# Optimization experiments

Hardware: AMD Instinct MI355X
Metric: run time of the kernel (lower is better)

## Reference

```python
import jax, jax.numpy as jnp
import numpy as np

N_NODES = 100000
N_EDGES = 1000000
S = 64      # n_hidden_scalars
F = 64      # n_hidden_edge_feats
RBF = 16    # rbf_dim
V = 16      # n_vec_channels
IN_DIM = 2 * S + F + RBF  # 208, EdgeUpdate MLP input


def _layernorm(x, g, b):
    m = x.mean(-1, keepdims=True)
    var = ((x - m) ** 2).mean(-1, keepdims=True)
    return (x - m) / jnp.sqrt(var + 1e-5) * g + b


def _gvp(s, v, Wh, Wu, Ws, bs, sigmoid_gate):
    # s: [N, S]; v: [N, v_in, 3]
    vh = jnp.einsum('nvc,vh->nhc', v, Wh)          # [N, h, 3]
    vu = jnp.einsum('nhc,hu->nuc', vh, Wu)          # [N, v_out, 3]
    sh = jnp.sqrt(jnp.sum(vh * vh, axis=-1) + 1e-8)  # [N, h]
    s_out = jax.nn.silu(jnp.concatenate([s, sh], axis=-1) @ Ws + bs)
    vn = jnp.sqrt(jnp.sum(vu * vu, axis=-1, keepdims=True) + 1e-8)  # [N, v_out, 1]
    gate = jax.nn.sigmoid(vn) if sigmoid_gate else vn
    return s_out, gate * vu


def setup_inputs() -> dict:
    key = jax.random.key(0)
    ks = jax.random.split(key, 24)

    def nrm(k, shape, fan_in):
        return jax.random.normal(k, shape, dtype=jnp.float32) / np.sqrt(fan_in)

    inp = {
        'node_scalars': jax.random.normal(ks[0], (N_NODES, S), dtype=jnp.float32),
        'positions': jax.random.normal(ks[1], (N_NODES, 3), dtype=jnp.float32),
        'vectors': jax.random.normal(ks[2], (N_NODES, V, 3), dtype=jnp.float32),
        'edge_feats': jax.random.normal(ks[3], (N_EDGES, F), dtype=jnp.float32),
        'd': jax.random.uniform(ks[4], (N_EDGES, RBF), dtype=jnp.float32),
        'src_idx': jax.random.randint(ks[5], (N_EDGES,), 0, N_NODES, dtype=jnp.int32),
        'dst_idx': jax.random.randint(ks[6], (N_EDGES,), 0, N_NODES, dtype=jnp.int32),
        # EdgeUpdate MLP + LayerNorm params
        'W1': nrm(ks[7], (IN_DIM, F), IN_DIM), 'b1': jnp.zeros((F,), jnp.float32),
        'W2': nrm(ks[8], (F, F), F),           'b2': jnp.zeros((F,), jnp.float32),
        'ln_g': jnp.ones((F,), jnp.float32),   'ln_b': jnp.zeros((F,), jnp.float32),
        # GVP 0: s 64->64, v 16->16 (h=16), sigmoid vector gate
        'gvp0_Wh': nrm(ks[9], (V, V), V), 'gvp0_Wu': nrm(ks[10], (V, V), V),
        'gvp0_Ws': nrm(ks[11], (S + V, S), S + V), 'gvp0_bs': jnp.zeros((S,), jnp.float32),
        # GVP 1: same shapes
        'gvp1_Wh': nrm(ks[12], (V, V), V), 'gvp1_Wu': nrm(ks[13], (V, V), V),
        'gvp1_Ws': nrm(ks[14], (S + V, S), S + V), 'gvp1_bs': jnp.zeros((S,), jnp.float32),
        # GVP 2 (last): v 16->1, identity vector activation
        'gvp2_Wh': nrm(ks[15], (V, V), V), 'gvp2_Wu': nrm(ks[16], (V, 1), V),
        'gvp2_Ws': nrm(ks[17], (S + V, S), S + V), 'gvp2_bs': jnp.zeros((S,), jnp.float32),
    }
    return inp


def reference(node_scalars, positions, vectors, edge_feats, d, src_idx, dst_idx,
              W1, b1, W2, b2, ln_g, ln_b,
              gvp0_Wh, gvp0_Wu, gvp0_Ws, gvp0_bs,
              gvp1_Wh, gvp1_Wu, gvp1_Ws, gvp1_bs,
              gvp2_Wh, gvp2_Wu, gvp2_Ws, gvp2_bs):
    # ---- EdgeUpdate: gather-concat-MLP + residual + LayerNorm ----
    h = jnp.concatenate(
        [node_scalars[src_idx], node_scalars[dst_idx], edge_feats, d], axis=-1)  # [E, 208]
    h = jax.nn.silu(h @ W1 + b1)
    h = jax.nn.silu(h @ W2 + b2)
    edge_out = _layernorm(edge_feats + h, ln_g, ln_b)  # [E, F]

    # ---- NodePositionUpdate: 3 stacked GVPs, last emits 1 vector channel ----
    s, v = node_scalars, vectors
    s, v = _gvp(s, v, gvp0_Wh, gvp0_Wu, gvp0_Ws, gvp0_bs, sigmoid_gate=True)
    s, v = _gvp(s, v, gvp1_Wh, gvp1_Wu, gvp1_Ws, gvp1_bs, sigmoid_gate=True)
    s, v = _gvp(s, v, gvp2_Wh, gvp2_Wu, gvp2_Ws, gvp2_bs, sigmoid_gate=False)  # v: [N,1,3]
    pos_out = positions + v[:, 0, :]  # [N, 3]

    return edge_out, pos_out
```

## Files before the change

kernel.cpp:

```cpp
#include <hip/hip_runtime.h>
#include <hip/hip_bf16.h>

#define N_NODES 100000
#define N_EDGES 1000000
#define S_DIM 64
#define F_DIM 64
#define RBF_DIM 16
#define V_CH 16

typedef __attribute__((ext_vector_type(4))) float f32x4;
typedef __attribute__((ext_vector_type(8))) short bf16x8;

#define NBLK 128
#define TPW 5
#define EDGE_GRID 3125

#define LDS_FENCE() asm volatile("" ::: "memory")

__device__ __forceinline__ float silu_f(float x) {
    return x * (1.0f / (1.0f + __expf(-x)));
}

__device__ __forceinline__ ushort f2bf(float x) {
    uint u = __float_as_uint(x);
    uint r = (u + 0x7fffu + ((u >> 16) & 1u)) >> 16;
    return (ushort)r;
}

__device__ __forceinline__ float4 ld4(const float* p) {
    return *reinterpret_cast<const float4*>(p);
}

__device__ __forceinline__ bf16x8 pack8(float4 u, float4 v) {
    bf16x8 r;
    r[0] = (short)f2bf(u.x); r[1] = (short)f2bf(u.y);
    r[2] = (short)f2bf(u.z); r[3] = (short)f2bf(u.w);
    r[4] = (short)f2bf(v.x); r[5] = (short)f2bf(v.y);
    r[6] = (short)f2bf(v.z); r[7] = (short)f2bf(v.w);
    return r;
}

struct Raw { float4 v[14]; };

__global__ __launch_bounds__(256, 2) void edge_kernel(
    const float* __restrict__ ns, const float* __restrict__ ef,
    const float* __restrict__ dd, const int* __restrict__ src,
    const int* __restrict__ dst, const float* __restrict__ W1,
    const float* __restrict__ b1, const float* __restrict__ W2,
    const float* __restrict__ b2, const float* __restrict__ lng,
    const float* __restrict__ lnb, float* __restrict__ out)
{
    __shared__ __align__(16) ushort b1f[7][4][64][8];
    __shared__ __align__(16) ushort b2f[2][4][64][8];
    __shared__ __align__(16) float  h2buf[4][16][68];

    const int tid  = threadIdx.x;
    const int lane = tid & 63;
    const int wid  = tid >> 6;
    const int l15  = lane & 15;
    const int g    = lane >> 4;

    {
        const int fl  = tid & 63;
        const int fnn = tid >> 6;
        const int col = 16 * fnn + (fl & 15);
        const int krow = (fl >> 4) << 3;
        #pragma unroll
        for (int kk = 0; kk < 7; ++kk) {
            const int k0 = 32 * kk + krow;
            bf16x8 w;
            #pragma unroll
            for (int j = 0; j < 8; ++j) {
                const int k = k0 + j;
                w[j] = (k < 208) ? (short)f2bf(W1[k * 64 + col]) : (short)0;
            }
            *reinterpret_cast<bf16x8*>(&b1f[kk][fnn][fl][0]) = w;
        }
        #pragma unroll
        for (int kk = 0; kk < 2; ++kk) {
            const int k0 = 32 * kk + krow;
            bf16x8 w;
            #pragma unroll
            for (int j = 0; j < 8; ++j) w[j] = (short)f2bf(W2[(k0 + j) * 64 + col]);
            *reinterpret_cast<bf16x8*>(&b2f[kk][fnn][fl][0]) = w;
        }
    }
    __syncthreads();

    float b1c[4], b2c[4], lgc[4], lbc[4];
    #pragma unroll
    for (int nn = 0; nn < 4; ++nn) {
        b1c[nn] = b1[16 * nn + l15];
        b2c[nn] = b2[16 * nn + l15];
        lgc[nn] = lng[16 * nn + l15];
        lbc[nn] = lnb[16 * nn + l15];
    }

    const int wtile0 = (blockIdx.x * 4 + wid) * TPW;

    int sis[TPW], dis[TPW];
    #pragma unroll
    for (int t = 0; t < TPW; ++t) {
        const int erow = (wtile0 + t) * 16 + l15;
        sis[t] = src[erow];
        dis[t] = dst[erow];
    }

    float (*hb)[68] = h2buf[wid];

    auto load_raw = [&](Raw& r, int t) {
        const int erow = (wtile0 + t) * 16 + l15;
        const float* ps = ns + (size_t)sis[t] * 64 + 8 * g;
        const float* pd = ns + (size_t)dis[t] * 64 + 8 * g;
        const float* pe = ef + (size_t)erow * 64 + 8 * g;
        const float* pr = dd + (size_t)erow * 16 + 8 * g;
        r.v[0] = ld4(ps);       r.v[1] = ld4(ps + 4);
        r.v[2] = ld4(ps + 32);  r.v[3] = ld4(ps + 36);
        r.v[4] = ld4(pd);       r.v[5] = ld4(pd + 4);
        r.v[6] = ld4(pd + 32);  r.v[7] = ld4(pd + 36);
        r.v[8] = ld4(pe);       r.v[9] = ld4(pe + 4);
        r.v[10] = ld4(pe + 32); r.v[11] = ld4(pe + 36);
        if (g < 2) { r.v[12] = ld4(pr); r.v[13] = ld4(pr + 4); }
        else { r.v[12] = make_float4(0.f,0.f,0.f,0.f); r.v[13] = make_float4(0.f,0.f,0.f,0.f); }
    };

    auto process = [&](const Raw& r, int t) {
        const int ebase = (wtile0 + t) * 16;

        bf16x8 a0 = pack8(r.v[0], r.v[1]);
        bf16x8 a1 = pack8(r.v[2], r.v[3]);
        bf16x8 a2f = pack8(r.v[4], r.v[5]);
        bf16x8 a3 = pack8(r.v[6], r.v[7]);
        bf16x8 a4 = pack8(r.v[8], r.v[9]);
        bf16x8 a5 = pack8(r.v[10], r.v[11]);
        bf16x8 a6 = pack8(r.v[12], r.v[13]);
        const float4 pef0 = r.v[8], pef1 = r.v[9], pef2 = r.v[10], pef3 = r.v[11];

        f32x4 acc[4];
        #pragma unroll
        for (int nn = 0; nn < 4; ++nn) acc[nn] = (f32x4){0.f, 0.f, 0.f, 0.f};
        #pragma unroll
        for (int nn = 0; nn < 4; ++nn) {
            acc[nn] = __builtin_amdgcn_mfma_f32_16x16x32_bf16(a0, *reinterpret_cast<const bf16x8*>(&b1f[0][nn][lane][0]), acc[nn], 0, 0, 0);
            acc[nn] = __builtin_amdgcn_mfma_f32_16x16x32_bf16(a1, *reinterpret_cast<const bf16x8*>(&b1f[1][nn][lane][0]), acc[nn], 0, 0, 0);
            acc[nn] = __builtin_amdgcn_mfma_f32_16x16x32_bf16(a2f, *reinterpret_cast<const bf16x8*>(&b1f[2][nn][lane][0]), acc[nn], 0, 0, 0);
            acc[nn] = __builtin_amdgcn_mfma_f32_16x16x32_bf16(a3, *reinterpret_cast<const bf16x8*>(&b1f[3][nn][lane][0]), acc[nn], 0, 0, 0);
            acc[nn] = __builtin_amdgcn_mfma_f32_16x16x32_bf16(a4, *reinterpret_cast<const bf16x8*>(&b1f[4][nn][lane][0]), acc[nn], 0, 0, 0);
            acc[nn] = __builtin_amdgcn_mfma_f32_16x16x32_bf16(a5, *reinterpret_cast<const bf16x8*>(&b1f[5][nn][lane][0]), acc[nn], 0, 0, 0);
            acc[nn] = __builtin_amdgcn_mfma_f32_16x16x32_bf16(a6, *reinterpret_cast<const bf16x8*>(&b1f[6][nn][lane][0]), acc[nn], 0, 0, 0);
        }

        LDS_FENCE();
        #pragma unroll
        for (int nn = 0; nn < 4; ++nn)
            #pragma unroll
            for (int rr = 0; rr < 4; ++rr)
                hb[4 * g + rr][16 * nn + l15] = silu_f(acc[nn][rr] + b1c[nn]);
        LDS_FENCE();
        bf16x8 q0, q1;
        #pragma unroll
        for (int j = 0; j < 8; ++j) {
            q0[j] = (short)f2bf(hb[l15][8 * g + j]);
            q1[j] = (short)f2bf(hb[l15][32 + 8 * g + j]);
        }
        LDS_FENCE();

        #pragma unroll
        for (int j = 0; j < 4; ++j) {
            hb[l15][8 * g + j]          = (&pef0.x)[j];
            hb[l15][8 * g + 4 + j]      = (&pef1.x)[j];
            hb[l15][32 + 8 * g + j]     = (&pef2.x)[j];
            hb[l15][32 + 8 * g + 4 + j] = (&pef3.x)[j];
        }

        f32x4 acc2[4];
        #pragma unroll
        for (int nn = 0; nn < 4; ++nn) acc2[nn] = (f32x4){0.f, 0.f, 0.f, 0.f};
        #pragma unroll
        for (int nn = 0; nn < 4; ++nn) {
            acc2[nn] = __builtin_amdgcn_mfma_f32_16x16x32_bf16(q0, *reinterpret_cast<const bf16x8*>(&b2f[0][nn][lane][0]), acc2[nn], 0, 0, 0);
            acc2[nn] = __builtin_amdgcn_mfma_f32_16x16x32_bf16(q1, *reinterpret_cast<const bf16x8*>(&b2f[1][nn][lane][0]), acc2[nn], 0, 0, 0);
        }

        LDS_FENCE();
        float x[4][4];
        #pragma unroll
        for (int nn = 0; nn < 4; ++nn)
            #pragma unroll
            for (int rr = 0; rr < 4; ++rr)
                x[nn][rr] = silu_f(acc2[nn][rr] + b2c[nn]) + hb[4 * g + rr][16 * nn + l15];

        float mean[4], rsd[4];
        #pragma unroll
        for (int rr = 0; rr < 4; ++rr) {
            float s = x[0][rr] + x[1][rr] + x[2][rr] + x[3][rr];
            s += __shfl_xor(s, 1); s += __shfl_xor(s, 2);
            s += __shfl_xor(s, 4); s += __shfl_xor(s, 8);
            mean[rr] = s * (1.0f / 64.0f);
        }
        #pragma unroll
        for (int rr = 0; rr < 4; ++rr) {
            float v = 0.f;
            #pragma unroll
            for (int nn = 0; nn < 4; ++nn) {
                const float dx = x[nn][rr] - mean[rr];
                v += dx * dx;
            }
            v += __shfl_xor(v, 1); v += __shfl_xor(v, 2);
            v += __shfl_xor(v, 4); v += __shfl_xor(v, 8);
            rsd[rr] = rsqrtf(v * (1.0f / 64.0f) + 1e-5f);
        }

        LDS_FENCE();
        #pragma unroll
        for (int nn = 0; nn < 4; ++nn)
            #pragma unroll
            for (int rr = 0; rr < 4; ++rr)
                hb[4 * g + rr][16 * nn + l15] =
                    (x[nn][rr] - mean[rr]) * rsd[rr] * lgc[nn] + lbc[nn];
        LDS_FENCE();

        float* obase = out + (size_t)ebase * 64;
        #pragma unroll
        for (int j = 0; j < 4; ++j) {
            const float* hr = &hb[4 * j + g][4 * l15];
            const float4 o = make_float4(hr[0], hr[1], hr[2], hr[3]);
            *reinterpret_cast<float4*>(obase + (size_t)(4 * j + g) * 64 + 4 * l15) = o;
        }
    };

    Raw rA, rB;
    load_raw(rA, 0);
    #pragma unroll
    for (int t = 0; t < TPW; ++t) {
        if (t & 1) {
            if (t < TPW - 1) load_raw(rA, t + 1);
            process(rB, t);
        } else {
            if (t < TPW - 1) load_raw(rB, t + 1);
            process(rA, t);
        }
    }
}

template <int UOUT, bool SIG>
__device__ __forceinline__ void gvp_step(
    float* __restrict__ s, float* __restrict__ vv,
    const float* __restrict__ Wh, const float* __restrict__ Wu,
    const float* __restrict__ Ws, const float* __restrict__ bs,
    float (*cat)[NBLK], const int tid)
{
    #pragma unroll
    for (int j = 0; j < 64; ++j) cat[j][tid] = s[j];

    float vu[UOUT * 3];
    #pragma unroll
    for (int i = 0; i < UOUT * 3; ++i) vu[i] = 0.0f;

    for (int h = 0; h < V_CH; ++h) {
        float t0 = 0.0f, t1 = 0.0f, t2 = 0.0f;
        #pragma unroll
        for (int vi = 0; vi < V_CH; ++vi) {
            const float wv = Wh[vi * V_CH + h];
            t0 = fmaf(vv[vi * 3 + 0], wv, t0);
            t1 = fmaf(vv[vi * 3 + 1], wv, t1);
            t2 = fmaf(vv[vi * 3 + 2], wv, t2);
        }
        cat[64 + h][tid] = sqrtf(t0 * t0 + t1 * t1 + t2 * t2 + 1e-8f);
        #pragma unroll
        for (int u = 0; u < UOUT; ++u) {
            const float wu = Wu[h * UOUT + u];
            vu[u * 3 + 0] = fmaf(t0, wu, vu[u * 3 + 0]);
            vu[u * 3 + 1] = fmaf(t1, wu, vu[u * 3 + 1]);
            vu[u * 3 + 2] = fmaf(t2, wu, vu[u * 3 + 2]);
        }
    }

    float acc[64];
    #pragma unroll
    for (int j = 0; j < 64; ++j) acc[j] = bs[j];
    #pragma unroll 2
    for (int k = 0; k < 64 + V_CH; ++k) {
        const float hk = cat[k][tid];
        const float* w = Ws + (size_t)k * 64;
        #pragma unroll
        for (int j = 0; j < 64; ++j) acc[j] = fmaf(hk, w[j], acc[j]);
    }
    #pragma unroll
    for (int j = 0; j < 64; ++j) s[j] = silu_f(acc[j]);

    #pragma unroll
    for (int u = 0; u < UOUT; ++u) {
        const float a = vu[u * 3 + 0];
        const float b = vu[u * 3 + 1];
        const float c = vu[u * 3 + 2];
        const float vn = sqrtf(a * a + b * b + c * c + 1e-8f);
        const float gt = SIG ? (1.0f / (1.0f + __expf(-vn))) : vn;
        vv[u * 3 + 0] = gt * a;
        vv[u * 3 + 1] = gt * b;
        vv[u * 3 + 2] = gt * c;
    }
}

__global__ __launch_bounds__(NBLK, 2) void node_kernel(
    const float* __restrict__ ns, const float* __restrict__ pos,
    const float* __restrict__ vec,
    const float* __restrict__ Wh0, const float* __restrict__ Wu0,
    const float* __restrict__ Ws0, const float* __restrict__ bs0,
    const float* __restrict__ Wh1, const float* __restrict__ Wu1,
    const float* __restrict__ Ws1, const float* __restrict__ bs1,
    const float* __restrict__ Wh2, const float* __restrict__ Wu2,
    const float* __restrict__ Ws2, const float* __restrict__ bs2,
    float* __restrict__ outpos)
{
    __shared__ float cat[64 + V_CH][NBLK];
    const int tid = threadIdx.x;
    const int n = blockIdx.x * NBLK + tid;
    const bool active = (n < N_NODES);
    const int nc = active ? n : 0;

    float s[64];
    {
        const float* p = ns + (size_t)nc * S_DIM;
        #pragma unroll
        for (int i = 0; i < 16; ++i) {
            float4 v4 = *reinterpret_cast<const float4*>(p + 4 * i);
            s[4 * i] = v4.x; s[4 * i + 1] = v4.y; s[4 * i + 2] = v4.z; s[4 * i + 3] = v4.w;
        }
    }
    float vv[48];
    {
        const float* p = vec + (size_t)nc * (V_CH * 3);
        #pragma unroll
        for (int i = 0; i < 12; ++i) {
            float4 v4 = *reinterpret_cast<const float4*>(p + 4 * i);
            vv[4 * i] = v4.x; vv[4 * i + 1] = v4.y; vv[4 * i + 2] = v4.z; vv[4 * i + 3] = v4.w;
        }
    }

    gvp_step<V_CH, true>(s, vv, Wh0, Wu0, Ws0, bs0, cat, tid);
    gvp_step<V_CH, true>(s, vv, Wh1, Wu1, Ws1, bs1, cat, tid);
    gvp_step<1, false>(s, vv, Wh2, Wu2, Ws2, bs2, cat, tid);

    if (active) {
        outpos[(size_t)n * 3 + 0] = pos[(size_t)n * 3 + 0] + vv[0];
        outpos[(size_t)n * 3 + 1] = pos[(size_t)n * 3 + 1] + vv[1];
        outpos[(size_t)n * 3 + 2] = pos[(size_t)n * 3 + 2] + vv[2];
    }
}

extern "C" void kernel_launch(void* const* d_in, const int* in_sizes, int n_in,
                              void* d_out, int out_size, void* d_ws, size_t ws_size,
                              hipStream_t stream) {
    const float* ns  = (const float*)d_in[0];
    const float* pos = (const float*)d_in[1];
    const float* vec = (const float*)d_in[2];
    const float* ef  = (const float*)d_in[3];
    const float* dd  = (const float*)d_in[4];
    const int*   src = (const int*)d_in[5];
    const int*   dst = (const int*)d_in[6];
    const float* W1  = (const float*)d_in[7];
    const float* b1  = (const float*)d_in[8];
    const float* W2  = (const float*)d_in[9];
    const float* b2  = (const float*)d_in[10];
    const float* lng = (const float*)d_in[11];
    const float* lnb = (const float*)d_in[12];
    const float* Wh0 = (const float*)d_in[13];
    const float* Wu0 = (const float*)d_in[14];
    const float* Ws0 = (const float*)d_in[15];
    const float* bs0 = (const float*)d_in[16];
    const float* Wh1 = (const float*)d_in[17];
    const float* Wu1 = (const float*)d_in[18];
    const float* Ws1 = (const float*)d_in[19];
    const float* bs1 = (const float*)d_in[20];
    const float* Wh2 = (const float*)d_in[21];
    const float* Wu2 = (const float*)d_in[22];
    const float* Ws2 = (const float*)d_in[23];
    const float* bs2 = (const float*)d_in[24];

    float* out     = (float*)d_out;
    float* out_pos = out + (size_t)N_EDGES * F_DIM;

    edge_kernel<<<EDGE_GRID, 256, 0, stream>>>(
        ns, ef, dd, src, dst, W1, b1, W2, b2, lng, lnb, out);
    node_kernel<<<(N_NODES + NBLK - 1) / NBLK, NBLK, 0, stream>>>(
        ns, pos, vec, Wh0, Wu0, Ws0, bs0, Wh1, Wu1, Ws1, bs1, Wh2, Wu2, Ws2, bs2, out_pos);
}
```

Baseline: 311.7 us.

## Restructure edge kernel epilogue, hold W2 in registers, single-buffer loads for occupancy

Replaces the two-register-buffer prefetch with a single Raw buffer that is reloaded right after packing. W2 fragments now live in registers instead of LDS. The layernorm epilogue now works in row-major layout: it re-reads edge_feats from global (likely L2-cached) and writes output straight from registers, which removes an LDS round trip. Launch bounds rise to 3 blocks per SM and f2bf uses the HIP intrinsic. The aim is higher occupancy and less LDS traffic, at the cost of an extra global read of edge_feats and register pressure from the 8 W2 fragments.

```diff
diff --git a/kernel.cpp b/kernel.cpp
--- a/kernel.cpp
+++ b/kernel.cpp
@@ -22,9 +22,9 @@
 }
 
 __device__ __forceinline__ ushort f2bf(float x) {
-    uint u = __float_as_uint(x);
-    uint r = (u + 0x7fffu + ((u >> 16) & 1u)) >> 16;
-    return (ushort)r;
+    union { __hip_bfloat16 b; ushort u; } c;
+    c.b = __float2bfloat16(x);
+    return c.u;
 }
 
 __device__ __forceinline__ float4 ld4(const float* p) {
@@ -42,7 +42,7 @@
 
 struct Raw { float4 v[14]; };
 
-__global__ __launch_bounds__(256, 2) void edge_kernel(
+__global__ __launch_bounds__(256, 3) void edge_kernel(
     const float* __restrict__ ns, const float* __restrict__ ef,
     const float* __restrict__ dd, const int* __restrict__ src,
     const int* __restrict__ dst, const float* __restrict__ W1,
@@ -51,8 +51,7 @@
     const float* __restrict__ lnb, float* __restrict__ out)
 {
     __shared__ __align__(16) ushort b1f[7][4][64][8];
-    __shared__ __align__(16) ushort b2f[2][4][64][8];
-    __shared__ __align__(16) float  h2buf[4][16][68];
+    __shared__ __align__(16) float  hb[4][16][68];
 
     const int tid  = threadIdx.x;
     const int lane = tid & 63;
@@ -76,25 +75,26 @@
             }
             *reinterpret_cast<bf16x8*>(&b1f[kk][fnn][fl][0]) = w;
         }
-        #pragma unroll
-        for (int kk = 0; kk < 2; ++kk) {
-            const int k0 = 32 * kk + krow;
-            bf16x8 w;
-            #pragma unroll
-            for (int j = 0; j < 8; ++j) w[j] = (short)f2bf(W2[(k0 + j) * 64 + col]);
-            *reinterpret_cast<bf16x8*>(&b2f[kk][fnn][fl][0]) = w;
-        }
     }
     __syncthreads();
 
-    float b1c[4], b2c[4], lgc[4], lbc[4];
+    bf16x8 w2r[2][4];
+    #pragma unroll
+    for (int kk = 0; kk < 2; ++kk)
+        #pragma unroll
+        for (int nn = 0; nn < 4; ++nn)
+            #pragma unroll
+            for (int j = 0; j < 8; ++j)
+                w2r[kk][nn][j] = (short)f2bf(W2[(32 * kk + 8 * g + j) * 64 + 16 * nn + l15]);
+
+    float b1c[4], b2c[4];
     #pragma unroll
     for (int nn = 0; nn < 4; ++nn) {
         b1c[nn] = b1[16 * nn + l15];
         b2c[nn] = b2[16 * nn + l15];
-        lgc[nn] = lng[16 * nn + l15];
-        lbc[nn] = lnb[16 * nn + l15];
-    }
+    }
+    const float4 lgq = ld4(lng + 4 * l15);
+    const float4 lbq = ld4(lnb + 4 * l15);
 
     const int wtile0 = (blockIdx.x * 4 + wid) * TPW;
 
@@ -106,7 +106,7 @@
         dis[t] = dst[erow];
     }
 
-    float (*hb)[68] = h2buf[wid];
+    float (*hbw)[68] = hb[wid];
 
     auto load_raw = [&](Raw& r, int t) {
         const int erow = (wtile0 + t) * 16 + l15;
@@ -124,7 +124,11 @@
         else { r.v[12] = make_float4(0.f,0.f,0.f,0.f); r.v[13] = make_float4(0.f,0.f,0.f,0.f); }
     };
 
-    auto process = [&](const Raw& r, int t) {
+    Raw r;
+    load_raw(r, 0);
+
+    #pragma unroll
+    for (int t = 0; t < TPW; ++t) {
         const int ebase = (wtile0 + t) * 16;
 
         bf16x8 a0 = pack8(r.v[0], r.v[1]);
@@ -134,7 +138,8 @@
         bf16x8 a4 = pack8(r.v[8], r.v[9]);
         bf16x8 a5 = pack8(r.v[10], r.v[11]);
         bf16x8 a6 = pack8(r.v[12], r.v[13]);
-        const float4 pef0 = r.v[8], pef1 = r.v[9], pef2 = r.v[10], pef3 = r.v[11];
+
+        if (t < TPW - 1) load_raw(r, t + 1);
 
         f32x4 acc[4];
         #pragma unroll
@@ -155,90 +160,65 @@
         for (int nn = 0; nn < 4; ++nn)
             #pragma unroll
             for (int rr = 0; rr < 4; ++rr)
-                hb[4 * g + rr][16 * nn + l15] = silu_f(acc[nn][rr] + b1c[nn]);
+                hbw[4 * g + rr][16 * nn + l15] = silu_f(acc[nn][rr] + b1c[nn]);
         LDS_FENCE();
         bf16x8 q0, q1;
         #pragma unroll
         for (int j = 0; j < 8; ++j) {
-            q0[j] = (short)f2bf(hb[l15][8 * g + j]);
-            q1[j] = (short)f2bf(hb[l15][32 + 8 * g + j]);
-        }
+            q0[j] = (short)f2bf(hbw[l15][8 * g + j]);
+            q1[j] = (short)f2bf(hbw[l15][32 + 8 * g + j]);
+        }
+
+        f32x4 acc2[4];
+        #pragma unroll
+        for (int nn = 0; nn < 4; ++nn) acc2[nn] = (f32x4){0.f, 0.f, 0.f, 0.f};
+        #pragma unroll
+        for (int nn = 0; nn < 4; ++nn) {
+            acc2[nn] = __builtin_amdgcn_mfma_f32_16x16x32_bf16(q0, w2r[0][nn], acc2[nn], 0, 0, 0);
+            acc2[nn] = __builtin_amdgcn_mfma_f32_16x16x32_bf16(q1, w2r[1][nn], acc2[nn], 0, 0, 0);
+        }
+
         LDS_FENCE();
-
+        #pragma unroll
+        for (int nn = 0; nn < 4; ++nn)
+            #pragma unroll
+            for (int rr = 0; rr < 4; ++rr)
+                hbw[4 * g + rr][16 * nn + l15] = silu_f(acc2[nn][rr] + b2c[nn]);
+        LDS_FENCE();
+
+        float x[4][4];
         #pragma unroll
         for (int j = 0; j < 4; ++j) {
-            hb[l15][8 * g + j]          = (&pef0.x)[j];
-            hb[l15][8 * g + 4 + j]      = (&pef1.x)[j];
-            hb[l15][32 + 8 * g + j]     = (&pef2.x)[j];
-            hb[l15][32 + 8 * g + 4 + j] = (&pef3.x)[j];
-        }
-
-        f32x4 acc2[4];
-        #pragma unroll
-        for (int nn = 0; nn < 4; ++nn) acc2[nn] = (f32x4){0.f, 0.f, 0.f, 0.f};
-        #pragma unroll
-        for (int nn = 0; nn < 4; ++nn) {
-            acc2[nn] = __builtin_amdgcn_mfma_f32_16x16x32_bf16(q0, *reinterpret_cast<const bf16x8*>(&b2f[0][nn][lane][0]), acc2[nn], 0, 0, 0);
-            acc2[nn] = __builtin_amdgcn_mfma_f32_16x16x32_bf16(q1, *reinterpret_cast<const bf16x8*>(&b2f[1][nn][lane][0]), acc2[nn], 0, 0, 0);
-        }
-
-        LDS_FENCE();
-        float x[4][4];
-        #pragma unroll
-        for (int nn = 0; nn < 4; ++nn)
-            #pragma unroll
-            for (int rr = 0; rr < 4; ++rr)
-                x[nn][rr] = silu_f(acc2[nn][rr] + b2c[nn]) + hb[4 * g + rr][16 * nn + l15];
-
-        float mean[4], rsd[4];
-        #pragma unroll
-        for (int rr = 0; rr < 4; ++rr) {
-            float s = x[0][rr] + x[1][rr] + x[2][rr] + x[3][rr];
+            const float* hr = &hbw[4 * j + g][4 * l15];
+            const float4 e = ld4(ef + (size_t)(ebase + 4 * j + g) * 64 + 4 * l15);
+            x[j][0] = hr[0] + e.x;
+            x[j][1] = hr[1] + e.y;
+            x[j][2] = hr[2] + e.z;
+            x[j][3] = hr[3] + e.w;
+        }
+
+        #pragma unroll
+        for (int j = 0; j < 4; ++j) {
+            float s = x[j][0] + x[j][1] + x[j][2] + x[j][3];
             s += __shfl_xor(s, 1); s += __shfl_xor(s, 2);
             s += __shfl_xor(s, 4); s += __shfl_xor(s, 8);
-            mean[rr] = s * (1.0f / 64.0f);
-        }
-        #pragma unroll
-        for (int rr = 0; rr < 4; ++rr) {
+            const float mean = s * (1.0f / 64.0f);
             float v = 0.f;
             #pragma unroll
-            for (int nn = 0; nn < 4; ++nn) {
-                const float dx = x[nn][rr] - mean[rr];
+            for (int c = 0; c < 4; ++c) {
+                const float dx = x[j][c] - mean;
                 v += dx * dx;
             }
             v += __shfl_xor(v, 1); v += __shfl_xor(v, 2);
             v += __shfl_xor(v, 4); v += __shfl_xor(v, 8);
-            rsd[rr] = rsqrtf(v * (1.0f / 64.0f) + 1e-5f);
-        }
-
-        LDS_FENCE();
-        #pragma unroll
-        for (int nn = 0; nn < 4; ++nn)
-            #pragma unroll
-            for (int rr = 0; rr < 4; ++rr)
-                hb[4 * g + rr][16 * nn + l15] =
-                    (x[nn][rr] - mean[rr]) * rsd[rr] * lgc[nn] + lbc[nn];
-        LDS_FENCE();
-
-        float* obase = out + (size_t)ebase * 64;
-        #pragma unroll
-        for (int j = 0; j < 4; ++j) {
-            const float* hr = &hb[4 * j + g][4 * l15];
-            const float4 o = make_float4(hr[0], hr[1], hr[2], hr[3]);
-            *reinterpret_cast<float4*>(obase + (size_t)(4 * j + g) * 64 + 4 * l15) = o;
-        }
-    };
-
-    Raw rA, rB;
-    load_raw(rA, 0);
-    #pragma unroll
-    for (int t = 0; t < TPW; ++t) {
-        if (t & 1) {
-            if (t < TPW - 1) load_raw(rA, t + 1);
-            process(rB, t);
-        } else {
-            if (t < TPW - 1) load_raw(rB, t + 1);
-            process(rA, t);
+            const float rsd = rsqrtf(v * (1.0f / 64.0f) + 1e-5f);
+
+            float4 o;
+            o.x = (x[j][0] - mean) * rsd * lgq.x + lbq.x;
+            o.y = (x[j][1] - mean) * rsd * lgq.y + lbq.y;
+            o.z = (x[j][2] - mean) * rsd * lgq.z + lbq.z;
+            o.w = (x[j][3] - mean) * rsd * lgq.w + lbq.w;
+            *reinterpret_cast<float4*>(out + (size_t)(ebase + 4 * j + g) * 64 + 4 * l15) = o;
         }
     }
 }
```

New measurement: 490.9 us. +57.5%, slower.
